# Performance work log

Hardware: AMD Instinct MI355X
Metric: run time of the kernel (lower is better)

## Reference

```python
import math
import jax, jax.numpy as jnp
import numpy as np

NUM_HEADS = 16

def setup_inputs() -> dict:
    key = jax.random.key(0)
    k1, k2, k3, k4, k5 = jax.random.split(key, 5)
    B, S, D = 8, 4096, 1024
    x = jax.random.normal(k1, (B, S, D), dtype=jnp.float32)
    W_qkv = jax.random.normal(k2, (D, 3 * D), dtype=jnp.float32) * (1.0 / math.sqrt(D))
    b_qkv = jax.random.normal(k3, (3 * D,), dtype=jnp.float32) * 0.02
    W_out = jax.random.normal(k4, (D, D), dtype=jnp.float32) * (1.0 / math.sqrt(D))
    b_out = jax.random.normal(k5, (D,), dtype=jnp.float32) * 0.02
    return {"x": x, "W_qkv": W_qkv, "b_qkv": b_qkv, "W_out": W_out, "b_out": b_out}

def reference(x, W_qkv, b_qkv, W_out, b_out):
    B, S, D = x.shape
    H = NUM_HEADS
    hd = D // H
    scale = 1.0 / math.sqrt(hd)
    # QKV projection: (B,S,D) -> (B,S,3D), reshaped to (B,S,H,3*hd)
    qkv = (x @ W_qkv + b_qkv).reshape(B, S, H, 3 * hd)
    q, k, v = jnp.split(qkv, 3, axis=-1)  # each (B,S,H,hd)
    # Faithful to source: no head permute, so attention is across the H heads
    # at each (batch, seq) position. scores: (B,S,H,H)
    scores = jnp.einsum('bsqd,bskd->bsqk', q, k) * scale
    attn = jax.nn.softmax(scores, axis=-1)
    values = jnp.einsum('bsqk,bskd->bsqd', attn, v).reshape(B, S, D)
    return values @ W_out + b_out
```

## Files before the change

### kernel.cpp

```cpp
#include <hip/hip_runtime.h>
#include <hip/hip_bf16.h>

#define TOKENS   32768
#define DMODEL   1024
#define THREE_D  3072

using u16 = unsigned short;
typedef __attribute__((ext_vector_type(8))) short short8;
typedef __attribute__((ext_vector_type(4))) float f32x4;

__device__ __forceinline__ float bf2f(u16 u) {
  union { unsigned int i; float f; } v; v.i = ((unsigned int)u) << 16; return v.f;
}
__device__ __forceinline__ u16 f2bf(float f) {
  __hip_bfloat16 h = __float2bfloat16(f);
  return *reinterpret_cast<u16*>(&h);
}

__device__ __forceinline__ void gload_lds16(const u16* g, u16* l) {
  __builtin_amdgcn_global_load_lds((const __attribute__((address_space(1))) void*)g,
                                   (__attribute__((address_space(3))) void*)l,
                                   16, 0, 0);
}

__global__ __launch_bounds__(256) void convert_f32_bf16(const float* __restrict__ in,
                                                        u16* __restrict__ out, long n) {
  long i = ((long)blockIdx.x * 256 + threadIdx.x) * 4;
  if (i >= n) return;
  float4 v = *reinterpret_cast<const float4*>(in + i);
  ushort4 o;
  o.x = f2bf(v.x); o.y = f2bf(v.y); o.z = f2bf(v.z); o.w = f2bf(v.w);
  *reinterpret_cast<ushort4*>(out + i) = o;
}

__global__ __launch_bounds__(256) void transpose_convert(const float* __restrict__ in,
                                                         u16* __restrict__ out,
                                                         int R, int C) {
  __shared__ u16 tile[32][33];
  const int bc = blockIdx.x * 32;
  const int br = blockIdx.y * 32;
  const int tx = threadIdx.x & 31;
  const int ty = threadIdx.x >> 5;
  #pragma unroll
  for (int i = 0; i < 32; i += 8)
    tile[ty + i][tx] = f2bf(in[(long)(br + ty + i) * C + bc + tx]);
  __syncthreads();
  #pragma unroll
  for (int i = 0; i < 32; i += 8)
    out[(long)(bc + ty + i) * R + br + tx] = tile[tx][ty + i];
}

#define BM 256
#define BN 256
#define BK 64

#define VM6 asm volatile("s_waitcnt vmcnt(6)" ::: "memory")
#define VM0 asm volatile("s_waitcnt vmcnt(0)" ::: "memory")
#define VMN ((void)0)
#define NOSTAGE ((void)0)

#define STAGE_A(T, H)                                                          \
  { _Pragma("unroll") for (int j_ = 0; j_ < 2; j_++) {                         \
      const int lr_ = (H) * 128 + (wave * 2 + j_) * 8;                         \
      gload_lds16(A + (long)(bm + lr_ + sr) * a_stride + (long)(T) * a_grp + scol, \
                  &As[(T) & 1][lr_ * BK]);                                     \
  } }
#define STAGE_B(T, H)                                                          \
  { _Pragma("unroll") for (int j_ = 0; j_ < 2; j_++) {                         \
      const int lr_ = (H) * 128 + (wave * 2 + j_) * 8;                         \
      gload_lds16(BT + (long)(bn + lr_ + sr) * K + (T) * BK + scol,            \
                  &Bs[(T) & 1][lr_ * BK]);                                     \
  } }

#define PHASE(BUF, QR, QC, RDA, RDB, STAGE, VMW)                               \
  {                                                                            \
    if (RDA) {                                                                 \
      _Pragma("unroll") for (int mi = 0; mi < 2; mi++)                         \
        _Pragma("unroll") for (int kh = 0; kh < 2; kh++)                       \
          a[mi][kh] = *reinterpret_cast<const short8*>(                        \
              &As[BUF][((QR) * 128 + wrow + mi * 16 + lrow) * BK +             \
                       (((kh * 4 + quad) ^ xs) * 8)]);                         \
    }                                                                          \
    if (RDB) {                                                                 \
      _Pragma("unroll") for (int ni = 0; ni < 4; ni++)                         \
        _Pragma("unroll") for (int kh = 0; kh < 2; kh++)                       \
          b[ni][kh] = *reinterpret_cast<const short8*>(                        \
              &Bs[BUF][((QC) * 128 + wcol + ni * 16 + lrow) * BK +             \
                       (((kh * 4 + quad) ^ xs) * 8)]);                         \
    }                                                                          \
    STAGE;                                                                     \
    VMW;                                                                       \
    __builtin_amdgcn_s_barrier();                                              \
    asm volatile("s_waitcnt lgkmcnt(0)" ::: "memory");                         \
    __builtin_amdgcn_sched_barrier(0);                                         \
    __builtin_amdgcn_s_setprio(1);                                             \
    _Pragma("unroll") for (int mi = 0; mi < 2; mi++)                           \
      _Pragma("unroll") for (int ni = 0; ni < 4; ni++) {                       \
        acc[QR][QC][mi][ni] = __builtin_amdgcn_mfma_f32_16x16x32_bf16(         \
            a[mi][0], b[ni][0], acc[QR][QC][mi][ni], 0, 0, 0);                 \
        acc[QR][QC][mi][ni] = __builtin_amdgcn_mfma_f32_16x16x32_bf16(         \
            a[mi][1], b[ni][1], acc[QR][QC][mi][ni], 0, 0, 0);                 \
      }                                                                        \
    __builtin_amdgcn_s_setprio(0);                                             \
    __builtin_amdgcn_s_barrier();                                              \
    __builtin_amdgcn_sched_barrier(0);                                         \
  }

template <bool OUT_F32>
__global__ __launch_bounds__(512, 2) void gemm_bt_bias(
    const u16* __restrict__ A, const u16* __restrict__ BT,
    const float* __restrict__ bias, void* __restrict__ Cv,
    int M, int N, int K, long a_stride, int a_grp) {
  __shared__ alignas(16) u16 As[2][BM * BK];
  __shared__ alignas(16) u16 Bs[2][BN * BK];
  (void)M;

  const int cpx = gridDim.x >> 3;
  const int wg  = ((int)blockIdx.x & 7) * cpx + ((int)blockIdx.x >> 3);
  const int tiles_n = N / BN;
  const int bm = (wg / tiles_n) * BM;
  const int bn = (wg % tiles_n) * BN;

  const int tid  = threadIdx.x;
  const int wave = tid >> 6;
  const int lane = tid & 63;
  const int wrow = (wave & 3) * 32;
  const int wcol = (wave >> 2) * 64;
  const int lrow = lane & 15;
  const int quad = lane >> 4;
  const int xs   = lrow & 7;

  const int sr     = lane >> 3;
  const int schunk = (lane & 7) ^ sr;
  const int scol   = schunk * 8;

  const int NT = K / BK;

  f32x4 acc[2][2][2][4];
  #pragma unroll
  for (int i = 0; i < 2; i++)
    #pragma unroll
    for (int j = 0; j < 2; j++)
      #pragma unroll
      for (int m = 0; m < 2; m++)
        #pragma unroll
        for (int n = 0; n < 4; n++) acc[i][j][m][n] = (f32x4){0.f, 0.f, 0.f, 0.f};

  STAGE_A(0, 0); STAGE_B(0, 0); STAGE_A(0, 1); STAGE_B(0, 1);
  STAGE_B(1, 0); STAGE_A(1, 1); STAGE_B(1, 1);
  VM6;
  __builtin_amdgcn_s_barrier();

  short8 a[2][2];
  short8 b[4][2];
  #pragma unroll 1
  for (int t = 0; t + 3 < NT; t += 2) {
    PHASE(0, 0, 0, 1, 1, STAGE_A(t + 1, 0), VMN);
    PHASE(0, 1, 0, 1, 0, STAGE_B(t + 2, 0), VMN);
    PHASE(0, 1, 1, 0, 1, STAGE_A(t + 2, 1), VMN);
    PHASE(0, 0, 1, 1, 0, STAGE_B(t + 2, 1), VM6);
    PHASE(1, 0, 0, 1, 1, STAGE_A(t + 2, 0), VMN);
    PHASE(1, 1, 0, 1, 0, STAGE_B(t + 3, 0), VMN);
    PHASE(1, 1, 1, 0, 1, STAGE_A(t + 3, 1), VMN);
    PHASE(1, 0, 1, 1, 0, STAGE_B(t + 3, 1), VM6);
  }
  PHASE(0, 0, 0, 1, 1, STAGE_A(NT - 1, 0), VMN);
  PHASE(0, 1, 0, 1, 0, NOSTAGE, VMN);
  PHASE(0, 1, 1, 0, 1, NOSTAGE, VMN);
  PHASE(0, 0, 1, 1, 0, NOSTAGE, VM0);
  PHASE(1, 0, 0, 1, 1, NOSTAGE, VMN);
  PHASE(1, 1, 0, 1, 0, NOSTAGE, VMN);
  PHASE(1, 1, 1, 0, 1, NOSTAGE, VMN);
  PHASE(1, 0, 1, 1, 0, NOSTAGE, VMN);

  #pragma unroll
  for (int qc = 0; qc < 2; qc++) {
    #pragma unroll
    for (int ni = 0; ni < 4; ni++) {
      const int col = bn + qc * 128 + wcol + ni * 16 + lrow;
      const float bv = bias[col];
      #pragma unroll
      for (int qr = 0; qr < 2; qr++) {
        #pragma unroll
        for (int mi = 0; mi < 2; mi++) {
          #pragma unroll
          for (int r = 0; r < 4; r++) {
            const int row = bm + qr * 128 + wrow + mi * 16 + quad * 4 + r;
            const float val = acc[qr][qc][mi][ni][r] + bv;
            if (OUT_F32)
              ((float*)Cv)[(long)row * N + col] = val;
            else
              ((u16*)Cv)[(long)row * N + col] = f2bf(val);
          }
        }
      }
    }
  }
}

__global__ __launch_bounds__(256) void attn_local(u16* __restrict__ qkv) {
  __shared__ float p_s[4][16][16];
  const int tid  = threadIdx.x;
  const int wave = tid >> 6;
  const int lane = tid & 63;
  const int t    = blockIdx.x * 4 + wave;
  u16* row = qkv + (long)t * THREE_D;
  const int lrow = lane & 15;
  const int quad = lane >> 4;
  const int kq   = quad * 8;

  short8 a0 = *reinterpret_cast<const short8*>(row + lrow * 192 + kq);
  short8 a1 = *reinterpret_cast<const short8*>(row + lrow * 192 + 32 + kq);
  short8 b0 = *reinterpret_cast<const short8*>(row + lrow * 192 + 64 + kq);
  short8 b1 = *reinterpret_cast<const short8*>(row + lrow * 192 + 96 + kq);
  f32x4 s = {0.f, 0.f, 0.f, 0.f};
  s = __builtin_amdgcn_mfma_f32_16x16x32_bf16(a0, b0, s, 0, 0, 0);
  s = __builtin_amdgcn_mfma_f32_16x16x32_bf16(a1, b1, s, 0, 0, 0);

  const float scale = 0.125f;
  float p[4];
  #pragma unroll
  for (int r = 0; r < 4; r++) {
    float x = s[r] * scale;
    float m = x;
    #pragma unroll
    for (int mask = 1; mask < 16; mask <<= 1) m = fmaxf(m, __shfl_xor(m, mask));
    float e = __expf(x - m);
    float l = e;
    #pragma unroll
    for (int mask = 1; mask < 16; mask <<= 1) l += __shfl_xor(l, mask);
    p[r] = e / l;
  }
  #pragma unroll
  for (int r = 0; r < 4; r++) p_s[wave][quad * 4 + r][lrow] = p[r];
  __syncthreads();

  float o[16];
  #pragma unroll
  for (int i = 0; i < 16; i++) o[i] = 0.f;
  #pragma unroll
  for (int j = 0; j < 16; j++) {
    float vj = bf2f(row[j * 192 + 128 + lane]);
    #pragma unroll
    for (int i = 0; i < 16; i++) o[i] += p_s[wave][i][j] * vj;
  }
  #pragma unroll
  for (int i = 0; i < 16; i++)
    row[i * 192 + lane] = f2bf(o[i]);
}

extern "C" void kernel_launch(void* const* d_in, const int* in_sizes, int n_in,
                              void* d_out, int out_size, void* d_ws, size_t ws_size,
                              hipStream_t stream) {
  const float* x     = (const float*)d_in[0];
  const float* W_qkv = (const float*)d_in[1];
  const float* b_qkv = (const float*)d_in[2];
  const float* W_out = (const float*)d_in[3];
  const float* b_out = (const float*)d_in[4];
  float* out = (float*)d_out;

  char* ws = (char*)d_ws;
  u16* qkv   = (u16*)ws;  ws += (size_t)TOKENS * THREE_D * 2;
  u16* x_bf  = (u16*)ws;  ws += (size_t)TOKENS * DMODEL * 2;
  u16* wqkvT = (u16*)ws;  ws += (size_t)THREE_D * DMODEL * 2;
  u16* woutT = (u16*)ws;

  dim3 tb(256);
  dim3 gtb(512);
  convert_f32_bf16<<<dim3((TOKENS * DMODEL) / 1024), tb, 0, stream>>>(
      x, x_bf, (long)TOKENS * DMODEL);
  transpose_convert<<<dim3(THREE_D / 32, DMODEL / 32), tb, 0, stream>>>(W_qkv, wqkvT, DMODEL, THREE_D);
  transpose_convert<<<dim3(DMODEL / 32, DMODEL / 32), tb, 0, stream>>>(W_out, woutT, DMODEL, DMODEL);
  gemm_bt_bias<false><<<dim3((TOKENS / BM) * (THREE_D / BN)), gtb, 0, stream>>>(
      x_bf, wqkvT, b_qkv, qkv, TOKENS, THREE_D, DMODEL, (long)DMODEL, 64);
  attn_local<<<dim3(TOKENS / 4), tb, 0, stream>>>(qkv);
  gemm_bt_bias<true><<<dim3((TOKENS / BM) * (DMODEL / BN)), gtb, 0, stream>>>(
      qkv, woutT, b_out, out, TOKENS, DMODEL, DMODEL, (long)THREE_D, 192);
}
```

Baseline: 599.6 us.

## Restructure GEMM main loop to prefetch next LDS fragments after MFMA, one barrier per phase

Reorders each phase of the bf16 GEMM pipeline so the LDS fragment reads for the next quadrant are issued after the current MFMA block, not before it, with the quadrant visiting order changed to a snake pattern to maximize fragment reuse. The trailing s_barrier of each phase is removed, leaving one barrier per region, and the vmcnt wait points move (VM4 in the third region instead of VM6 in the fourth). The goal is to hide LDS read latency and halve barrier overhead. The cost is that correctness now depends on careful buffer-reuse ordering without the second barrier, which risks races and adds register pressure.

After: 617.4 us. 3.0% more time.

```diff
diff --git a/kernel.cpp b/kernel.cpp
--- a/kernel.cpp
+++ b/kernel.cpp
@@ -54,6 +54,7 @@
 #define BN 256
 #define BK 64
 
+#define VM4 asm volatile("s_waitcnt vmcnt(4)" ::: "memory")
 #define VM6 asm volatile("s_waitcnt vmcnt(6)" ::: "memory")
 #define VM0 asm volatile("s_waitcnt vmcnt(0)" ::: "memory")
 #define VMN ((void)0)
@@ -72,24 +73,22 @@
                   &Bs[(T) & 1][lr_ * BK]);                                     \
   } }
 
-#define PHASE(BUF, QR, QC, RDA, RDB, STAGE, VMW)                               \
+#define READ_A(BUF, QR)                                                        \
+  { _Pragma("unroll") for (int mi = 0; mi < 2; mi++)                           \
+      _Pragma("unroll") for (int kh = 0; kh < 2; kh++)                         \
+        a[mi][kh] = *reinterpret_cast<const short8*>(                          \
+            &As[BUF][((QR) * 128 + wrow + mi * 16 + lrow) * BK +               \
+                     (((kh * 4 + quad) ^ xs) * 8)]); }
+#define READ_B(BUF, QC)                                                        \
+  { _Pragma("unroll") for (int ni = 0; ni < 4; ni++)                           \
+      _Pragma("unroll") for (int kh = 0; kh < 2; kh++)                         \
+        b[ni][kh] = *reinterpret_cast<const short8*>(                          \
+            &Bs[BUF][((QC) * 128 + wcol + ni * 16 + lrow) * BK +               \
+                     (((kh * 4 + quad) ^ xs) * 8)]); }
+
+#define REGION(QR, QC, STAGE, READS, VMW)                                      \
   {                                                                            \
-    if (RDA) {                                                                 \
-      _Pragma("unroll") for (int mi = 0; mi < 2; mi++)                         \
-        _Pragma("unroll") for (int kh = 0; kh < 2; kh++)                       \
-          a[mi][kh] = *reinterpret_cast<const short8*>(                        \
-              &As[BUF][((QR) * 128 + wrow + mi * 16 + lrow) * BK +             \
-                       (((kh * 4 + quad) ^ xs) * 8)]);                         \
-    }                                                                          \
-    if (RDB) {                                                                 \
-      _Pragma("unroll") for (int ni = 0; ni < 4; ni++)                         \
-        _Pragma("unroll") for (int kh = 0; kh < 2; kh++)                       \
-          b[ni][kh] = *reinterpret_cast<const short8*>(                        \
-              &Bs[BUF][((QC) * 128 + wcol + ni * 16 + lrow) * BK +             \
-                       (((kh * 4 + quad) ^ xs) * 8)]);                         \
-    }                                                                          \
-    STAGE;                                                                     \
-    VMW;                                                                       \
+    __builtin_amdgcn_sched_barrier(0);                                         \
     __builtin_amdgcn_s_barrier();                                              \
     asm volatile("s_waitcnt lgkmcnt(0)" ::: "memory");                         \
     __builtin_amdgcn_sched_barrier(0);                                         \
@@ -102,8 +101,9 @@
             a[mi][1], b[ni][1], acc[QR][QC][mi][ni], 0, 0, 0);                 \
       }                                                                        \
     __builtin_amdgcn_s_setprio(0);                                             \
-    __builtin_amdgcn_s_barrier();                                              \
-    __builtin_amdgcn_sched_barrier(0);                                         \
+    STAGE;                                                                     \
+    READS;                                                                     \
+    VMW;                                                                       \
   }
 
 template <bool OUT_F32>
@@ -153,25 +153,28 @@
 
   short8 a[2][2];
   short8 b[4][2];
+  READ_A(0, 0);
+  READ_B(0, 0);
+
   #pragma unroll 1
   for (int t = 0; t + 3 < NT; t += 2) {
-    PHASE(0, 0, 0, 1, 1, STAGE_A(t + 1, 0), VMN);
-    PHASE(0, 1, 0, 1, 0, STAGE_B(t + 2, 0), VMN);
-    PHASE(0, 1, 1, 0, 1, STAGE_A(t + 2, 1), VMN);
-    PHASE(0, 0, 1, 1, 0, STAGE_B(t + 2, 1), VM6);
-    PHASE(1, 0, 0, 1, 1, STAGE_A(t + 2, 0), VMN);
-    PHASE(1, 1, 0, 1, 0, STAGE_B(t + 3, 0), VMN);
-    PHASE(1, 1, 1, 0, 1, STAGE_A(t + 3, 1), VMN);
-    PHASE(1, 0, 1, 1, 0, STAGE_B(t + 3, 1), VM6);
-  }
-  PHASE(0, 0, 0, 1, 1, STAGE_A(NT - 1, 0), VMN);
-  PHASE(0, 1, 0, 1, 0, NOSTAGE, VMN);
-  PHASE(0, 1, 1, 0, 1, NOSTAGE, VMN);
-  PHASE(0, 0, 1, 1, 0, NOSTAGE, VM0);
-  PHASE(1, 0, 0, 1, 1, NOSTAGE, VMN);
-  PHASE(1, 1, 0, 1, 0, NOSTAGE, VMN);
-  PHASE(1, 1, 1, 0, 1, NOSTAGE, VMN);
-  PHASE(1, 0, 1, 1, 0, NOSTAGE, VMN);
+    REGION(0, 0, STAGE_A(t + 1, 0), READ_A(0, 1),              VMN);
+    REGION(1, 0, STAGE_B(t + 2, 0), READ_B(0, 1),              VMN);
+    REGION(1, 1, STAGE_A(t + 2, 1), READ_A(0, 0),              VM4);
+    REGION(0, 1, STAGE_B(t + 2, 1), { READ_A(1, 0) READ_B(1, 0) }, VMN);
+    REGION(0, 0, STAGE_A(t + 2, 0), READ_A(1, 1),              VMN);
+    REGION(1, 0, STAGE_B(t + 3, 0), READ_B(1, 1),              VMN);
+    REGION(1, 1, STAGE_A(t + 3, 1), READ_A(1, 0),              VM4);
+    REGION(0, 1, STAGE_B(t + 3, 1), { READ_A(0, 0) READ_B(0, 0) }, VMN);
+  }
+  REGION(0, 0, STAGE_A(NT - 1, 0), READ_A(0, 1),               VMN);
+  REGION(1, 0, NOSTAGE,            READ_B(0, 1),               VMN);
+  REGION(1, 1, NOSTAGE,            READ_A(0, 0),               VM0);
+  REGION(0, 1, NOSTAGE,            { READ_A(1, 0) READ_B(1, 0) }, VMN);
+  REGION(0, 0, NOSTAGE,            READ_A(1, 1),               VMN);
+  REGION(1, 0, NOSTAGE,            READ_B(1, 1),               VMN);
+  REGION(1, 1, NOSTAGE,            READ_A(1, 0),               VMN);
+  REGION(0, 1, NOSTAGE,            NOSTAGE,                    VMN);
 
   #pragma unroll
   for (int qc = 0; qc < 2; qc++) {
```
